# Kernel tuning notes

Hardware: AMD Instinct MI355X
Metric: run time of the kernel (lower is better)

The kernel has to match this reference:

```python
import jax, jax.numpy as jnp
import numpy as np

N = 100000   # nodes
E = 1600000  # edges (avg degree 16)
IN = 128
HID = 128


def _init_params(key):
    ks = jax.random.split(key, 3)
    def glorot(k, fan_in, fan_out):
        s = (6.0 / (fan_in + fan_out)) ** 0.5
        return jax.random.uniform(k, (fan_in, fan_out), jnp.float32, -s, s)
    W1 = glorot(ks[0], IN, HID)
    W_mu = glorot(ks[1], HID, HID)
    W_lv = glorot(ks[2], HID, HID)
    b1 = jnp.zeros((HID,), jnp.float32)
    b_mu = jnp.zeros((HID,), jnp.float32)
    b_lv = jnp.zeros((HID,), jnp.float32)
    return W1, b1, W_mu, b_mu, W_lv, b_lv


def setup_inputs() -> dict:
    key = jax.random.key(0)
    k_x, k_e, k_p = jax.random.split(key, 3)
    x = jax.random.normal(k_x, (N, IN), jnp.float32)
    edge_index = jax.random.randint(k_e, (2, E), 0, N, jnp.int32)
    W1, b1, W_mu, b_mu, W_lv, b_lv = _init_params(k_p)
    return {"x": x, "edge_index": edge_index,
            "W1": W1, "b1": b1, "W_mu": W_mu, "b_mu": b_mu,
            "W_lv": W_lv, "b_lv": b_lv}


def _gcn_conv(x, src, dst, coef, self_coef, W, b):
    # PyG GCNConv: h = X W;  out_i = sum_j norm_ji * h_j  (incl. self loop) + b
    h = x @ W                                   # [N, H] dense GEMM
    msg = h[src] * coef[:, None]                # gather + scale  [E, H]
    agg = jnp.zeros_like(h).at[dst].add(msg)    # scatter-add      [N, H]
    agg = agg + h * self_coef[:, None]          # self-loop contribution
    return agg + b


def reference(x, edge_index, W1, b1, W_mu, b_mu, W_lv, b_lv):
    src, dst = edge_index[0], edge_index[1]
    n = x.shape[0]
    # symmetric norm with self loops: deg_i = in_degree_i + 1
    deg = jnp.zeros((n,), x.dtype).at[dst].add(1.0) + 1.0
    dinv = jax.lax.rsqrt(deg)
    coef = dinv[src] * dinv[dst]                # per-edge norm
    self_coef = dinv * dinv                     # per-node self-loop norm

    h = jax.nn.elu(_gcn_conv(x, src, dst, coef, self_coef, W1, b1))
    mu = _gcn_conv(h, src, dst, coef, self_coef, W_mu, b_mu)
    logvar = _gcn_conv(h, src, dst, coef, self_coef, W_lv, b_lv)

    # reparameterize: z = mu + eps * exp(0.5*logvar)
    eps = jax.random.normal(jax.random.key(42), mu.shape, mu.dtype)
    z = mu + eps * jnp.exp(0.5 * logvar)
    return z, mu, logvar
```

## Files before the change

### kernel.cpp

```cpp
#include <hip/hip_runtime.h>
#include <hip/hip_bf16.h>
#include <cstring>
#include <cstdint>

#define N_NODES 100000
#define N_EDGES 1600000
#define HID 128
#define TOT (N_NODES * HID)
#define GEMM_GRID_C 782
#define SCAT_GRID_C 6250



typedef __bf16 bf16x8 __attribute__((ext_vector_type(8)));
typedef float f32x4 __attribute__((ext_vector_type(4)));

__device__ __forceinline__ float2 ld2(const float* p) { return *(const float2*)p; }
__device__ __forceinline__ float2 ld2(const __hip_bfloat16* p) {
    const __hip_bfloat162 h = *(const __hip_bfloat162*)p;
    return make_float2(__bfloat162float(h.x), __bfloat162float(h.y));
}

__device__ __forceinline__ void store8(float* p, const float* v) {
    *(float4*)(p)     = make_float4(v[0], v[1], v[2], v[3]);
    *(float4*)(p + 4) = make_float4(v[4], v[5], v[6], v[7]);
}
__device__ __forceinline__ void store8(__hip_bfloat16* p, const float* v) {
    union { unsigned short us[8]; uint4 q; } u;
#pragma unroll
    for (int i = 0; i < 8; ++i) {
        __hip_bfloat16 b = __float2bfloat16(v[i]);
        unsigned short raw;
        memcpy(&raw, &b, 2);
        u.us[i] = raw;
    }
    *(uint4*)p = u.q;
}

__global__ void k_count_rank(const int* __restrict__ dst, int* __restrict__ counts,
                             int* __restrict__ rank) {
    int e = blockIdx.x * 256 + threadIdx.x;
    if (e < N_EDGES) rank[e] = atomicAdd(&counts[dst[e]], 1);
}

__global__ void k_scan_block(const int* __restrict__ counts, int* __restrict__ partial,
                             int* __restrict__ bsum) {
    __shared__ int s[256];
    int i = blockIdx.x * 256 + threadIdx.x;
    int v = (i < N_NODES) ? counts[i] : 0;
    s[threadIdx.x] = v;
    __syncthreads();
    for (int off = 1; off < 256; off <<= 1) {
        int t = (threadIdx.x >= off) ? s[threadIdx.x - off] : 0;
        __syncthreads();
        s[threadIdx.x] += t;
        __syncthreads();
    }
    if (i < N_NODES) partial[i] = s[threadIdx.x] - v;
    if (threadIdx.x == 255) bsum[blockIdx.x] = s[255];
}

__global__ void k_scan_sums(int* __restrict__ bsum, int nb) {
    __shared__ int s[512];
    int v = (threadIdx.x < nb) ? bsum[threadIdx.x] : 0;
    s[threadIdx.x] = v;
    __syncthreads();
    for (int off = 1; off < 512; off <<= 1) {
        int t = (threadIdx.x >= off) ? s[threadIdx.x - off] : 0;
        __syncthreads();
        s[threadIdx.x] += t;
        __syncthreads();
    }
    if (threadIdx.x < nb) bsum[threadIdx.x] = s[threadIdx.x] - v;
}

__global__ void k_finalize(const int* __restrict__ counts, const int* __restrict__ partial,
                           const int* __restrict__ bsum, int* __restrict__ offsets,
                           float* __restrict__ dinv) {
    int i = blockIdx.x * 256 + threadIdx.x;
    if (i < N_NODES) {
        int o = partial[i] + bsum[blockIdx.x];
        offsets[i] = o;
        dinv[i] = rsqrtf((float)(counts[i] + 1));
    }
    if (i == 0) offsets[N_NODES] = N_EDGES;
}

__global__ void k_prep_w(const float* __restrict__ Wmu, const float* __restrict__ Wlv,
                         __hip_bfloat16* __restrict__ wmu_t,
                         __hip_bfloat16* __restrict__ wlv_t) {
    int idx = blockIdx.x * 256 + threadIdx.x;
    if (idx < 128 * 128) {
        int k = idx >> 7, n = idx & 127;
        wmu_t[n * 128 + k] = __float2bfloat16(Wmu[idx]);
        wlv_t[n * 128 + k] = __float2bfloat16(Wlv[idx]);
    }
}

__global__ __launch_bounds__(256) void k_gemm1_scatter(
    const float* __restrict__ A, const float* __restrict__ W,
    __hip_bfloat16* __restrict__ out,
    const int* __restrict__ src, const int* __restrict__ dst,
    const int* __restrict__ rank, const int* __restrict__ offsets,
    const float* __restrict__ dinv, int2* __restrict__ sorted) {
    __shared__ float Wl[16][128];
    __shared__ float Al[128][16];

    if (blockIdx.x >= GEMM_GRID_C) {
        int e = (blockIdx.x - GEMM_GRID_C) * 256 + threadIdx.x;
        if (e < N_EDGES) {
            int s = src[e], d = dst[e];
            int pos = offsets[d] + rank[e];
            float c = dinv[s] * dinv[d];
            sorted[pos] = make_int2(s, __float_as_int(c));
        }
        return;
    }

    int t = threadIdx.x;
    int R = blockIdx.x * 128;
    int tx = t & 15, ty = t >> 4;
    int c0 = tx * 8;
    int r0 = ty * 8;
    float acc[8][8] = {};

    for (int k0 = 0; k0 < 128; k0 += 16) {
        {
            const float4* Wg = (const float4*)(W + k0 * 128);
            ((float4*)&Wl[0][0])[t] = Wg[t];
            ((float4*)&Wl[0][0])[t + 256] = Wg[t + 256];
        }
        {
#pragma unroll
            for (int ii = 0; ii < 2; ++ii) {
                int id = t + ii * 256;
                int row = id >> 2, c4 = (id & 3) * 4;
                int gr = R + row;
                float4 v = make_float4(0.f, 0.f, 0.f, 0.f);
                if (gr < N_NODES) v = *(const float4*)(A + (size_t)gr * HID + k0 + c4);
                *(float4*)(&Al[row][c4]) = v;
            }
        }
        __syncthreads();

#pragma unroll
        for (int kk4 = 0; kk4 < 4; ++kk4) {
            float4 av4[8];
#pragma unroll
            for (int j = 0; j < 8; ++j) av4[j] = *(const float4*)(&Al[r0 + j][kk4 * 4]);
            const float* av = (const float*)av4;
#pragma unroll
            for (int kk = 0; kk < 4; ++kk) {
                float4 b0 = *(const float4*)(&Wl[kk4 * 4 + kk][c0]);
                float4 b1 = *(const float4*)(&Wl[kk4 * 4 + kk][c0 + 4]);
#pragma unroll
                for (int j = 0; j < 8; ++j) {
                    float a = av[j * 4 + kk];
                    acc[j][0] = fmaf(a, b0.x, acc[j][0]);
                    acc[j][1] = fmaf(a, b0.y, acc[j][1]);
                    acc[j][2] = fmaf(a, b0.z, acc[j][2]);
                    acc[j][3] = fmaf(a, b0.w, acc[j][3]);
                    acc[j][4] = fmaf(a, b1.x, acc[j][4]);
                    acc[j][5] = fmaf(a, b1.y, acc[j][5]);
                    acc[j][6] = fmaf(a, b1.z, acc[j][6]);
                    acc[j][7] = fmaf(a, b1.w, acc[j][7]);
                }
            }
        }
        __syncthreads();
    }

#pragma unroll
    for (int j = 0; j < 8; ++j) {
        int gr = R + r0 + j;
        if (gr >= N_NODES) continue;
        float v[8];
#pragma unroll
        for (int c = 0; c < 8; ++c) v[c] = acc[j][c];
        store8(out + (size_t)gr * HID + c0, v);
    }
}

#define AGG_BATCH(U)                                                              \
    {                                                                             \
        int2 sv[U];                                                               \
        float2 xs[U];                                                             \
        _Pragma("unroll") for (int i = 0; i < U; ++i) sv[i] = sorted[e + i];      \
        _Pragma("unroll") for (int i = 0; i < U; ++i)                             \
            xs[i] = ld2(Xf + (size_t)sv[i].x * HID);                              \
        _Pragma("unroll") for (int i = 0; i < U; ++i) {                           \
            float c = __int_as_float(sv[i].y);                                    \
            a0 = fmaf(c, xs[i].x, a0);                                            \
            a1 = fmaf(c, xs[i].y, a1);                                            \
        }                                                                         \
        e += U;                                                                   \
    }

#define AGG_BATCH_CLAMPED(U)                                                      \
    {                                                                             \
        int2 sv[U];                                                               \
        float2 xs[U];                                                             \
        _Pragma("unroll") for (int i = 0; i < U; ++i) {                           \
            int ee = e + i;                                                       \
            sv[i] = sorted[(ee < e1) ? ee : (e1 - 1)];                            \
        }                                                                         \
        _Pragma("unroll") for (int i = 0; i < U; ++i)                             \
            xs[i] = ld2(Xf + (size_t)sv[i].x * HID);                              \
        _Pragma("unroll") for (int i = 0; i < U; ++i) {                           \
            float c = (e + i < e1) ? __int_as_float(sv[i].y) : 0.f;               \
            a0 = fmaf(c, xs[i].x, a0);                                            \
            a1 = fmaf(c, xs[i].y, a1);                                            \
        }                                                                         \
    }

#define AGG_CORE(XTYPE)                                                           \
    int node = (blockIdx.x * 256 + threadIdx.x) >> 6;                             \
    int lane = threadIdx.x & 63;                                                  \
    if (node >= N_NODES) return;                                                  \
    int f = lane * 2;                                                             \
    const XTYPE* __restrict__ Xf = X + f;                                         \
    float di = dinv[node];                                                        \
    float sc = di * di;                                                           \
    float2 xi = ld2(Xf + (size_t)node * HID);                                     \
    float a0 = sc * xi.x, a1 = sc * xi.y;                                         \
    int e = offsets[node], e1 = offsets[node + 1];                                \
    int rem = e1 - e;                                                             \
    while (rem >= 16) {                                                           \
        AGG_BATCH(16);                                                            \
        rem -= 16;                                                                \
    }                                                                             \
    if (rem > 8) {                                                                \
        AGG_BATCH_CLAMPED(16);                                                    \
    } else if (rem > 0) {                                                         \
        AGG_BATCH_CLAMPED(8);                                                     \
    }

__global__ __launch_bounds__(256) void k_agg_h(const __hip_bfloat16* __restrict__ X,
                                               const int* __restrict__ offsets,
                                               const int2* __restrict__ sorted,
                                               const float* __restrict__ dinv,
                                               const float* __restrict__ b1,
                                               __hip_bfloat16* __restrict__ out) {
    AGG_CORE(__hip_bfloat16)
    float v0 = a0 + b1[f];
    float v1 = a1 + b1[f + 1];
    v0 = (v0 > 0.f) ? v0 : expm1f(v0);
    v1 = (v1 > 0.f) ? v1 : expm1f(v1);
    __hip_bfloat162 hb;
    hb.x = __float2bfloat16(v0);
    hb.y = __float2bfloat16(v1);
    *(__hip_bfloat162*)(out + (size_t)node * HID + f) = hb;
}

__global__ __launch_bounds__(256) void k_agg_bf16(const __hip_bfloat16* __restrict__ X,
                                                  const int* __restrict__ offsets,
                                                  const int2* __restrict__ sorted,
                                                  const float* __restrict__ dinv,
                                                  __hip_bfloat16* __restrict__ out) {
    AGG_CORE(__hip_bfloat16)
    __hip_bfloat162 hb;
    hb.x = __float2bfloat16(a0);
    hb.y = __float2bfloat16(a1);
    *(__hip_bfloat162*)(out + (size_t)node * HID + f) = hb;
}

__global__ __launch_bounds__(256) void k_gemm_pair_mfma(
    const __hip_bfloat16* __restrict__ A,
    const __hip_bfloat16* __restrict__ wmu_t, const float* __restrict__ bmu,
    const __hip_bfloat16* __restrict__ wlv_t, const float* __restrict__ blv,
    float* __restrict__ mu, float* __restrict__ lv) {
    int which = (blockIdx.x >= GEMM_GRID_C);
    const __hip_bfloat16* __restrict__ wt = which ? wlv_t : wmu_t;
    const float* __restrict__ bias = which ? blv : bmu;
    float* __restrict__ out = which ? lv : mu;
    int bx = which ? (blockIdx.x - GEMM_GRID_C) : blockIdx.x;

    int w = threadIdx.x >> 6;
    int l = threadIdx.x & 63;
    int l16 = l & 15, lg = l >> 4;
    int wrow = bx * 128 + w * 32;

    bf16x8 a[2][4];
#pragma unroll
    for (int mt = 0; mt < 2; ++mt) {
#pragma unroll
        for (int ks = 0; ks < 4; ++ks) {
            int row = wrow + mt * 16 + l16;
            int rr = (row < N_NODES) ? row : (N_NODES - 1);
            a[mt][ks] = *reinterpret_cast<const bf16x8*>(
                A + (size_t)rr * HID + ks * 32 + lg * 8);
        }
    }

    f32x4 acc[2][8];
#pragma unroll
    for (int mt = 0; mt < 2; ++mt)
#pragma unroll
        for (int nt = 0; nt < 8; ++nt) acc[mt][nt] = (f32x4){0.f, 0.f, 0.f, 0.f};

#pragma unroll
    for (int nt = 0; nt < 8; ++nt) {
        bf16x8 b[4];
#pragma unroll
        for (int ks = 0; ks < 4; ++ks)
            b[ks] = *reinterpret_cast<const bf16x8*>(
                wt + (size_t)(nt * 16 + l16) * HID + ks * 32 + lg * 8);
#pragma unroll
        for (int ks = 0; ks < 4; ++ks) {
            acc[0][nt] = __builtin_amdgcn_mfma_f32_16x16x32_bf16(a[0][ks], b[ks],
                                                                acc[0][nt], 0, 0, 0);
            acc[1][nt] = __builtin_amdgcn_mfma_f32_16x16x32_bf16(a[1][ks], b[ks],
                                                                acc[1][nt], 0, 0, 0);
        }
    }

#pragma unroll
    for (int nt = 0; nt < 8; ++nt) {
        float bc = bias[nt * 16 + l16];
#pragma unroll
        for (int mt = 0; mt < 2; ++mt) {
#pragma unroll
            for (int r = 0; r < 4; ++r) {
                int gr = wrow + mt * 16 + lg * 4 + r;
                if (gr < N_NODES)
                    out[(size_t)gr * HID + nt * 16 + l16] = acc[mt][nt][r] + bc;
            }
        }
    }
}

__device__ __forceinline__ unsigned rotl32(unsigned x, int r) {
    return (x << r) | (x >> (32 - r));
}

__device__ __forceinline__ void threefry2x32(unsigned x0, unsigned x1, unsigned& o0,
                                             unsigned& o1) {
    const unsigned ks0 = 0u, ks1 = 42u, ks2 = 0x1BD11BDAu ^ 42u;
    x0 += ks0;
    x1 += ks1;
    x0 += x1; x1 = rotl32(x1, 13); x1 ^= x0;
    x0 += x1; x1 = rotl32(x1, 15); x1 ^= x0;
    x0 += x1; x1 = rotl32(x1, 26); x1 ^= x0;
    x0 += x1; x1 = rotl32(x1, 6);  x1 ^= x0;
    x0 += ks1; x1 += ks2 + 1u;
    x0 += x1; x1 = rotl32(x1, 17); x1 ^= x0;
    x0 += x1; x1 = rotl32(x1, 29); x1 ^= x0;
    x0 += x1; x1 = rotl32(x1, 16); x1 ^= x0;
    x0 += x1; x1 = rotl32(x1, 24); x1 ^= x0;
    x0 += ks2; x1 += ks0 + 2u;
    x0 += x1; x1 = rotl32(x1, 13); x1 ^= x0;
    x0 += x1; x1 = rotl32(x1, 15); x1 ^= x0;
    x0 += x1; x1 = rotl32(x1, 26); x1 ^= x0;
    x0 += x1; x1 = rotl32(x1, 6);  x1 ^= x0;
    x0 += ks0; x1 += ks1 + 3u;
    x0 += x1; x1 = rotl32(x1, 17); x1 ^= x0;
    x0 += x1; x1 = rotl32(x1, 29); x1 ^= x0;
    x0 += x1; x1 = rotl32(x1, 16); x1 ^= x0;
    x0 += x1; x1 = rotl32(x1, 24); x1 ^= x0;
    x0 += ks1; x1 += ks2 + 4u;
    x0 += x1; x1 = rotl32(x1, 13); x1 ^= x0;
    x0 += x1; x1 = rotl32(x1, 15); x1 ^= x0;
    x0 += x1; x1 = rotl32(x1, 26); x1 ^= x0;
    x0 += x1; x1 = rotl32(x1, 6);  x1 ^= x0;
    x0 += ks2; x1 += ks0 + 5u;
    o0 = x0;
    o1 = x1;
}

__device__ __forceinline__ float erfinv_f32(float x) {
    float w = -log1pf(-x * x);
    float p;
    if (w < 5.0f) {
        w -= 2.5f;
        p = 2.81022636e-08f;
        p = fmaf(p, w, 3.43273939e-07f);
        p = fmaf(p, w, -3.5233877e-06f);
        p = fmaf(p, w, -4.39150654e-06f);
        p = fmaf(p, w, 0.00021858087f);
        p = fmaf(p, w, -0.00125372503f);
        p = fmaf(p, w, -0.00417768164f);
        p = fmaf(p, w, 0.246640727f);
        p = fmaf(p, w, 1.50140941f);
    } else {
        w = sqrtf(w) - 3.0f;
        p = -0.000200214257f;
        p = fmaf(p, w, 0.000100950558f);
        p = fmaf(p, w, 0.00134934322f);
        p = fmaf(p, w, -0.00367342844f);
        p = fmaf(p, w, 0.00573950773f);
        p = fmaf(p, w, -0.0076224613f);
        p = fmaf(p, w, 0.00943887047f);
        p = fmaf(p, w, 1.00167406f);
        p = fmaf(p, w, 2.83297682f);
    }
    return p * x;
}

__global__ __launch_bounds__(256) void k_sample(const float* __restrict__ mu,
                                                const float* __restrict__ lv,
                                                float* __restrict__ z) {
    int j = blockIdx.x * 256 + threadIdx.x;
    if (j >= TOT) return;
    unsigned o0, o1;
    threefry2x32(0u, (unsigned)j, o0, o1);
    unsigned bits = o0 ^ o1;
    float f = __uint_as_float((bits >> 9) | 0x3f800000u) - 1.0f;
    float u = f * 2.0f - 0.99999994f;
    u = fmaxf(u, -0.99999994f);
    float eps = 1.41421356f * erfinv_f32(u);
    z[j] = fmaf(eps, expf(0.5f * lv[j]), mu[j]);
}

extern "C" void kernel_launch(void* const* d_in, const int* in_sizes, int n_in,
                              void* d_out, int out_size, void* d_ws, size_t ws_size,
                              hipStream_t stream) {
    const float* x = (const float*)d_in[0];
    const int* ei = (const int*)d_in[1];
    const float* W1 = (const float*)d_in[2];
    const float* b1 = (const float*)d_in[3];
    const float* Wmu = (const float*)d_in[4];
    const float* bmu = (const float*)d_in[5];
    const float* Wlv = (const float*)d_in[6];
    const float* blv = (const float*)d_in[7];

    float* z = (float*)d_out;
    float* mu = z + (size_t)TOT;
    float* lv = z + 2 * (size_t)TOT;

    char* ws = (char*)d_ws;
    __hip_bfloat16* t1buf = (__hip_bfloat16*)(ws + 0ull);
    __hip_bfloat16* habf = (__hip_bfloat16*)(ws + 0ull);
    int* rank = (int*)(ws + 25600000ull);
    __hip_bfloat16* hbf = (__hip_bfloat16*)(ws + 51200000ull);
    int* counts = (int*)(ws + 76800000ull);
    int* partial = (int*)(ws + 77200000ull);
    int* bsum = (int*)(ws + 77600000ull);
    int* offsets = (int*)(ws + 77602048ull);
    __hip_bfloat16* wmu_t = (__hip_bfloat16*)(ws + 78002176ull);
    __hip_bfloat16* wlv_t = (__hip_bfloat16*)(ws + 78034944ull);
    float* dinv = (float*)(ws + 78402176ull);
    int2* sorted = (int2*)(ws + 78802176ull);

    const int* src = ei;
    const int* dst = ei + N_EDGES;

    const int NBLK = (N_NODES + 255) / 256;
    const int AGG_GRID = (N_NODES * 64 + 255) / 256;

    hipMemsetAsync(counts, 0, N_NODES * sizeof(int), stream);
    k_prep_w<<<64, 256, 0, stream>>>(Wmu, Wlv, wmu_t, wlv_t);
    k_count_rank<<<SCAT_GRID_C, 256, 0, stream>>>(dst, counts, rank);
    k_scan_block<<<NBLK, 256, 0, stream>>>(counts, partial, bsum);
    k_scan_sums<<<1, 512, 0, stream>>>(bsum, NBLK);
    k_finalize<<<NBLK, 256, 0, stream>>>(counts, partial, bsum, offsets, dinv);

    k_gemm1_scatter<<<GEMM_GRID_C + SCAT_GRID_C, 256, 0, stream>>>(
        x, W1, t1buf, src, dst, rank, offsets, dinv, sorted);

    k_agg_h<<<AGG_GRID, 256, 0, stream>>>(t1buf, offsets, sorted, dinv, b1, hbf);

    k_agg_bf16<<<AGG_GRID, 256, 0, stream>>>(hbf, offsets, sorted, dinv, habf);
    k_gemm_pair_mfma<<<2 * GEMM_GRID_C, 256, 0, stream>>>(habf, wmu_t, bmu, wlv_t, blv,
                                                          mu, lv);

    k_sample<<<(TOT + 255) / 256, 256, 0, stream>>>(mu, lv, z);
}
```

Measured before the change: 585.6 us.

## Fuse mu/logvar GEMMs with reparameterization sampling via shared-memory staging

Merges the paired mu/logvar MFMA GEMM and the separate sampling kernel into one kernel. Each block computes both projections for a 16-column slice, stages them in LDS, then writes mu, logvar and z with coalesced stores. This avoids re-reading mu and logvar from global memory and saves a launch. The cost is halving the grid (782 blocks, each doing both GEMMs), an nt loop that is no longer unrolled, and extra barriers. The edge-sort scatter also switches to a packed 64-bit nontemporal store.

After: 638.6 us. 1.09x slower.

```diff
diff --git a/kernel.cpp b/kernel.cpp
--- a/kernel.cpp
+++ b/kernel.cpp
@@ -112,7 +112,10 @@
             int s = src[e], d = dst[e];
             int pos = offsets[d] + rank[e];
             float c = dinv[s] * dinv[d];
-            sorted[pos] = make_int2(s, __float_as_int(c));
+            unsigned long long v =
+                ((unsigned long long)(unsigned)__float_as_int(c) << 32) |
+                (unsigned long long)(unsigned)s;
+            __builtin_nontemporal_store(v, (unsigned long long*)(sorted + pos));
         }
         return;
     }
@@ -262,71 +265,6 @@
     hb.x = __float2bfloat16(a0);
     hb.y = __float2bfloat16(a1);
     *(__hip_bfloat162*)(out + (size_t)node * HID + f) = hb;
-}
-
-__global__ __launch_bounds__(256) void k_gemm_pair_mfma(
-    const __hip_bfloat16* __restrict__ A,
-    const __hip_bfloat16* __restrict__ wmu_t, const float* __restrict__ bmu,
-    const __hip_bfloat16* __restrict__ wlv_t, const float* __restrict__ blv,
-    float* __restrict__ mu, float* __restrict__ lv) {
-    int which = (blockIdx.x >= GEMM_GRID_C);
-    const __hip_bfloat16* __restrict__ wt = which ? wlv_t : wmu_t;
-    const float* __restrict__ bias = which ? blv : bmu;
-    float* __restrict__ out = which ? lv : mu;
-    int bx = which ? (blockIdx.x - GEMM_GRID_C) : blockIdx.x;
-
-    int w = threadIdx.x >> 6;
-    int l = threadIdx.x & 63;
-    int l16 = l & 15, lg = l >> 4;
-    int wrow = bx * 128 + w * 32;
-
-    bf16x8 a[2][4];
-#pragma unroll
-    for (int mt = 0; mt < 2; ++mt) {
-#pragma unroll
-        for (int ks = 0; ks < 4; ++ks) {
-            int row = wrow + mt * 16 + l16;
-            int rr = (row < N_NODES) ? row : (N_NODES - 1);
-            a[mt][ks] = *reinterpret_cast<const bf16x8*>(
-                A + (size_t)rr * HID + ks * 32 + lg * 8);
-        }
-    }
-
-    f32x4 acc[2][8];
-#pragma unroll
-    for (int mt = 0; mt < 2; ++mt)
-#pragma unroll
-        for (int nt = 0; nt < 8; ++nt) acc[mt][nt] = (f32x4){0.f, 0.f, 0.f, 0.f};
-
-#pragma unroll
-    for (int nt = 0; nt < 8; ++nt) {
-        bf16x8 b[4];
-#pragma unroll
-        for (int ks = 0; ks < 4; ++ks)
-            b[ks] = *reinterpret_cast<const bf16x8*>(
-                wt + (size_t)(nt * 16 + l16) * HID + ks * 32 + lg * 8);
-#pragma unroll
-        for (int ks = 0; ks < 4; ++ks) {
-            acc[0][nt] = __builtin_amdgcn_mfma_f32_16x16x32_bf16(a[0][ks], b[ks],
-                                                                acc[0][nt], 0, 0, 0);
-            acc[1][nt] = __builtin_amdgcn_mfma_f32_16x16x32_bf16(a[1][ks], b[ks],
-                                                                acc[1][nt], 0, 0, 0);
-        }
-    }
-
-#pragma unroll
-    for (int nt = 0; nt < 8; ++nt) {
-        float bc = bias[nt * 16 + l16];
-#pragma unroll
-        for (int mt = 0; mt < 2; ++mt) {
-#pragma unroll
-            for (int r = 0; r < 4; ++r) {
-                int gr = wrow + mt * 16 + lg * 4 + r;
-                if (gr < N_NODES)
-                    out[(size_t)gr * HID + nt * 16 + l16] = acc[mt][nt][r] + bc;
-            }
-        }
-    }
 }
 
 __device__ __forceinline__ unsigned rotl32(unsigned x, int r) {
@@ -396,19 +334,97 @@
     return p * x;
 }
 
-__global__ __launch_bounds__(256) void k_sample(const float* __restrict__ mu,
-                                                const float* __restrict__ lv,
-                                                float* __restrict__ z) {
-    int j = blockIdx.x * 256 + threadIdx.x;
-    if (j >= TOT) return;
+__device__ __forceinline__ float sample_eps(unsigned j) {
     unsigned o0, o1;
-    threefry2x32(0u, (unsigned)j, o0, o1);
+    threefry2x32(0u, j, o0, o1);
     unsigned bits = o0 ^ o1;
     float f = __uint_as_float((bits >> 9) | 0x3f800000u) - 1.0f;
     float u = f * 2.0f - 0.99999994f;
     u = fmaxf(u, -0.99999994f);
-    float eps = 1.41421356f * erfinv_f32(u);
-    z[j] = fmaf(eps, expf(0.5f * lv[j]), mu[j]);
+    return 1.41421356f * erfinv_f32(u);
+}
+
+__global__ __launch_bounds__(256) void k_gemm2_mfma_sample(
+    const __hip_bfloat16* __restrict__ A,
+    const __hip_bfloat16* __restrict__ wmu_t, const float* __restrict__ bmu,
+    const __hip_bfloat16* __restrict__ wlv_t, const float* __restrict__ blv,
+    float* __restrict__ mu, float* __restrict__ lv, float* __restrict__ z) {
+    __shared__ float Sm[128][17];
+    __shared__ float Sv[128][17];
+    int w = threadIdx.x >> 6;
+    int l = threadIdx.x & 63;
+    int l16 = l & 15, lg = l >> 4;
+    int bx = blockIdx.x;
+    int wrow = bx * 128 + w * 32;
+
+    bf16x8 a[2][4];
+#pragma unroll
+    for (int mt = 0; mt < 2; ++mt) {
+#pragma unroll
+        for (int ks = 0; ks < 4; ++ks) {
+            int row = wrow + mt * 16 + l16;
+            int rr = (row < N_NODES) ? row : (N_NODES - 1);
+            a[mt][ks] = *reinterpret_cast<const bf16x8*>(
+                A + (size_t)rr * HID + ks * 32 + lg * 8);
+        }
+    }
+
+#pragma unroll 1
+    for (int nt = 0; nt < 8; ++nt) {
+        f32x4 am0 = {0.f, 0.f, 0.f, 0.f}, am1 = {0.f, 0.f, 0.f, 0.f};
+        f32x4 al0 = {0.f, 0.f, 0.f, 0.f}, al1 = {0.f, 0.f, 0.f, 0.f};
+        {
+            bf16x8 b[4];
+#pragma unroll
+            for (int ks = 0; ks < 4; ++ks)
+                b[ks] = *reinterpret_cast<const bf16x8*>(
+                    wmu_t + (size_t)(nt * 16 + l16) * HID + ks * 32 + lg * 8);
+#pragma unroll
+            for (int ks = 0; ks < 4; ++ks) {
+                am0 = __builtin_amdgcn_mfma_f32_16x16x32_bf16(a[0][ks], b[ks], am0, 0, 0, 0);
+                am1 = __builtin_amdgcn_mfma_f32_16x16x32_bf16(a[1][ks], b[ks], am1, 0, 0, 0);
+            }
+        }
+        {
+            bf16x8 b[4];
+#pragma unroll
+            for (int ks = 0; ks < 4; ++ks)
+                b[ks] = *reinterpret_cast<const bf16x8*>(
+                    wlv_t + (size_t)(nt * 16 + l16) * HID + ks * 32 + lg * 8);
+#pragma unroll
+            for (int ks = 0; ks < 4; ++ks) {
+                al0 = __builtin_amdgcn_mfma_f32_16x16x32_bf16(a[0][ks], b[ks], al0, 0, 0, 0);
+                al1 = __builtin_amdgcn_mfma_f32_16x16x32_bf16(a[1][ks], b[ks], al1, 0, 0, 0);
+            }
+        }
+        float bm = bmu[nt * 16 + l16];
+        float bv = blv[nt * 16 + l16];
+#pragma unroll
+        for (int r = 0; r < 4; ++r) {
+            Sm[w * 32 + lg * 4 + r][l16] = am0[r] + bm;
+            Sm[w * 32 + 16 + lg * 4 + r][l16] = am1[r] + bm;
+            Sv[w * 32 + lg * 4 + r][l16] = al0[r] + bv;
+            Sv[w * 32 + 16 + lg * 4 + r][l16] = al1[r] + bv;
+        }
+        __syncthreads();
+#pragma unroll 1
+        for (int it = 0; it < 8; ++it) {
+            int idx = it * 256 + threadIdx.x;
+            int row = idx >> 4, c16 = idx & 15;
+            int gr = bx * 128 + row;
+            if (gr < N_NODES) {
+                float m = Sm[row][c16];
+                float lval = Sv[row][c16];
+                int col = nt * 16 + c16;
+                float eps = sample_eps((unsigned)(gr * 128 + col));
+                size_t o = (size_t)gr * HID + col;
+                mu[o] = m;
+                lv[o] = lval;
+                z[o] = fmaf(eps, expf(0.5f * lval), m);
+            }
+        }
+        __syncthreads();
+    }
 }
 
 extern "C" void kernel_launch(void* const* d_in, const int* in_sizes, int n_in,
@@ -460,8 +476,6 @@
     k_agg_h<<<AGG_GRID, 256, 0, stream>>>(t1buf, offsets, sorted, dinv, b1, hbf);
 
     k_agg_bf16<<<AGG_GRID, 256, 0, stream>>>(hbf, offsets, sorted, dinv, habf);
-    k_gemm_pair_mfma<<<2 * GEMM_GRID_C, 256, 0, stream>>>(habf, wmu_t, bmu, wlv_t, blv,
-                                                          mu, lv);
-
-    k_sample<<<(TOT + 255) / 256, 256, 0, stream>>>(mu, lv, z);
-}
+    k_gemm2_mfma_sample<<<GEMM_GRID_C, 256, 0, stream>>>(habf, wmu_t, bmu, wlv_t, blv,
+                                                         mu, lv, z);
+}
```
